# Kernel tuning notes

Measured on AMD Instinct MI355X. Metric: run time of the kernel, lower is better.

Reference implementation:

```python
import jax, jax.numpy as jnp
import numpy as np

B, PATCH, S, D, LAYERS, TOP_K, N_HEADS = 32, 196, 77, 512, 2, 16, 8


def setup_inputs() -> dict:
    key = jax.random.key(0)
    ks = jax.random.split(key, 16)
    d, L = D, LAYERS
    attn_std = d ** -0.5
    proj_std = (d ** -0.5) * ((2 * L) ** -0.5)
    fc_std = (2 * d) ** -0.5
    scale = d ** -0.5
    f = jnp.float32
    return {
        'image_feature': jax.random.normal(ks[0], (B, d), f),
        'image_tokens': jax.random.normal(ks[1], (B, PATCH, d), f),
        'text_feature': jax.random.normal(ks[2], (B, d), f),
        'text_tokens': jax.random.normal(ks[3], (B, S, d), f),
        'atte_mask': jax.random.randint(ks[4], (B, S), 0, 2).astype(jnp.int32),
        'img_cls': scale * jax.random.normal(ks[5], (d,), f),
        'txt_cls': scale * jax.random.normal(ks[6], (d,), f),
        'in_proj_w': attn_std * jax.random.normal(ks[7], (L, 3 * d, d), f),
        'in_proj_b': jnp.zeros((L, 3 * d), f),
        'out_w': proj_std * jax.random.normal(ks[8], (L, d, d), f),
        'out_b': jnp.zeros((L, d), f),
        'ln1_w': jnp.ones((L, d), f), 'ln1_b': jnp.zeros((L, d), f),
        'ln2_w': jnp.ones((L, d), f), 'ln2_b': jnp.zeros((L, d), f),
        'ln3_w': jnp.ones((L, d), f), 'ln3_b': jnp.zeros((L, d), f),
        'fc_w': fc_std * jax.random.normal(ks[9], (L, 4 * d, d), f),
        'fc_b': jnp.zeros((L, 4 * d), f),
        'proj_w': proj_std * jax.random.normal(ks[10], (L, d, 4 * d), f),
        'proj_b': jnp.zeros((L, d), f),
    }


def _ln(x, w, b):
    m = jnp.mean(x, axis=-1, keepdims=True)
    v = jnp.mean((x - m) ** 2, axis=-1, keepdims=True)
    return (x - m) * jax.lax.rsqrt(v + 1e-5) * w + b


def _mha(q, k, wi, bi, wo, bo):
    # q: (N, Lq, d), k: (N, Lk, d)
    N, Lq, d = q.shape
    hd = d // N_HEADS
    qh = (q @ wi[:d].T + bi[:d]).reshape(N, Lq, N_HEADS, hd)
    kh = (k @ wi[d:2 * d].T + bi[d:2 * d]).reshape(N, -1, N_HEADS, hd)
    vh = (k @ wi[2 * d:].T + bi[2 * d:]).reshape(N, -1, N_HEADS, hd)
    att = jax.nn.softmax(jnp.einsum('bqhd,bkhd->bhqk', qh, kh) * (hd ** -0.5), axis=-1)
    o = jnp.einsum('bhqk,bkhd->bqhd', att, vh).reshape(N, Lq, d)
    return o @ wo.T + bo


def _cross_attention(q4, k4, p):
    shape4 = q4.shape
    q = q4.reshape(-1, q4.shape[-2], q4.shape[-1])
    k = k4.reshape(-1, k4.shape[-2], k4.shape[-1])
    for i in range(LAYERS):
        kn = _ln(k, p['ln2_w'][i], p['ln2_b'][i])
        q = q + _mha(_ln(q, p['ln1_w'][i], p['ln1_b'][i]), kn,
                     p['in_proj_w'][i], p['in_proj_b'][i], p['out_w'][i], p['out_b'][i])
        h = _ln(q, p['ln3_w'][i], p['ln3_b'][i]) @ p['fc_w'][i].T + p['fc_b'][i]
        h = h * jax.nn.sigmoid(1.702 * h)  # QuickGELU
        q = q + h @ p['proj_w'][i].T + p['proj_b'][i]
    return q.reshape(shape4)


def _forward(image_feature, image_tokens, text_feature, text_tokens, atte_mask,
             img_cls, txt_cls, p):
    b, patch, d = image_tokens.shape
    s = text_tokens.shape[1]
    img_n = image_tokens / jnp.linalg.norm(image_tokens, axis=-1, keepdims=True)
    txt_n = text_tokens / jnp.linalg.norm(text_tokens, axis=-1, keepdims=True)
    # pairwise token similarities: (b_img, b_txt, patch, s)
    sim = jnp.einsum('ipd,jsd->ijps', img_n, txt_n)
    img_scores = jnp.einsum('ijps,js->ijp', sim, atte_mask.astype(sim.dtype))
    txt_scores = sim.sum(axis=2)  # (b, b, s)
    # top-k; torch scatter+masked_select gathers in ascending index order
    idx_i = jnp.sort(jax.lax.top_k(img_scores, TOP_K)[1], axis=-1)  # (b,b,k)
    idx_t = jnp.sort(jax.lax.top_k(txt_scores, TOP_K)[1], axis=-1)
    img_sel = img_n[jnp.arange(b)[:, None, None], idx_i]  # (b,b,k,d)
    txt_sel = txt_n[jnp.arange(b)[None, :, None], idx_t]  # (b,b,k,d)
    img_feat = jnp.broadcast_to(image_feature[:, None, None, :], (b, b, 1, d))
    txt_feat = jnp.broadcast_to(text_feature[None, :, None, :], (b, b, 1, d))
    img_cls4 = jnp.broadcast_to(img_cls, (b, b, 1, d))
    txt_cls4 = jnp.broadcast_to(txt_cls, (b, b, 1, d))
    final_img = _cross_attention(jnp.concatenate([img_cls4, img_sel], axis=2),
                                 jnp.concatenate([txt_feat, txt_sel], axis=2), p)
    final_txt = _cross_attention(jnp.concatenate([txt_cls4, txt_sel], axis=2),
                                 jnp.concatenate([img_feat, img_sel], axis=2), p)
    return final_img, final_txt


def reference(image_feature, image_tokens, text_feature, text_tokens, atte_mask,
              img_cls, txt_cls, in_proj_w, in_proj_b, out_w, out_b,
              ln1_w, ln1_b, ln2_w, ln2_b, ln3_w, ln3_b,
              fc_w, fc_b, proj_w, proj_b):
    p = dict(in_proj_w=in_proj_w, in_proj_b=in_proj_b, out_w=out_w, out_b=out_b,
             ln1_w=ln1_w, ln1_b=ln1_b, ln2_w=ln2_w, ln2_b=ln2_b,
             ln3_w=ln3_w, ln3_b=ln3_b, fc_w=fc_w, fc_b=fc_b,
             proj_w=proj_w, proj_b=proj_b)
    return _forward(image_feature, image_tokens, text_feature, text_tokens,
                    atte_mask, img_cls, txt_cls, p)
```

## Files before the change

### kernel.cpp

```cpp
#include <hip/hip_runtime.h>
#include <hip/hip_bf16.h>
#include <stdint.h>


typedef __attribute__((ext_vector_type(8))) short short8;
typedef __attribute__((ext_vector_type(4))) float f32x4;

__device__ __forceinline__ float bf2f(short u) {
    return __uint_as_float(((uint32_t)(uint16_t)u) << 16);
}
__device__ __forceinline__ unsigned short f2bf(float f) {
    __hip_bfloat16 h = __float2bfloat16(f);
    return *reinterpret_cast<unsigned short*>(&h);
}
__device__ __forceinline__ void gload16(const void* g, void* l) {
    __builtin_amdgcn_global_load_lds(
        (const __attribute__((address_space(1))) unsigned int*)g,
        (__attribute__((address_space(3))) unsigned int*)l, 16, 0, 0);
}

__global__ __launch_bounds__(256) void k_f2b(const float* __restrict__ in,
                                             unsigned short* __restrict__ out, int n) {
    for (int i = blockIdx.x * 256 + threadIdx.x; i < n; i += gridDim.x * 256)
        out[i] = f2bf(in[i]);
}

__global__ __launch_bounds__(256) void k_l2norm(const float* __restrict__ in,
                                                float* __restrict__ out) {
    size_t row = blockIdx.x;
    const float* x = in + row * 512;
    int t = threadIdx.x;
    float a0 = x[t], a1 = x[t + 256];
    float ss = a0 * a0 + a1 * a1;
#pragma unroll
    for (int off = 32; off; off >>= 1) ss += __shfl_xor(ss, off);
    __shared__ float s4[4];
    if ((t & 63) == 0) s4[t >> 6] = ss;
    __syncthreads();
    float tot = s4[0] + s4[1] + s4[2] + s4[3];
    float inv = 1.0f / sqrtf(tot);
    out[row * 512 + t] = a0 * inv;
    out[row * 512 + t + 256] = a1 * inv;
}

__global__ __launch_bounds__(512) void k_colsum(const float* __restrict__ tok,
                                                const int* __restrict__ mask,
                                                float* __restrict__ out, int R) {
    int b = blockIdx.x;
    int d = threadIdx.x;
    float acc = 0.f;
    for (int r = 0; r < R; r++) {
        float m = mask ? (float)mask[b * R + r] : 1.f;
        acc += m * tok[((size_t)b * R + r) * 512 + d];
    }
    out[b * 512 + d] = acc;
}

__global__ __launch_bounds__(256) void k_scores(const float* __restrict__ tok,
                                                const float* __restrict__ vec,
                                                float* __restrict__ out, int R, int swap) {
    int bid = blockIdx.x;
    int i = bid >> 5, j = bid & 31;
    int tb = swap ? j : i;
    int vb = swap ? i : j;
    __shared__ float sv[512];
    for (int t = threadIdx.x; t < 512; t += 256) sv[t] = vec[vb * 512 + t];
    __syncthreads();
    int wv = threadIdx.x >> 6, lane = threadIdx.x & 63;
    for (int r = wv; r < R; r += 4) {
        const float* tr = tok + ((size_t)tb * R + r) * 512;
        float acc = 0.f;
#pragma unroll
        for (int c = 0; c < 8; c++) {
            int d = lane + c * 64;
            acc += tr[d] * sv[d];
        }
#pragma unroll
        for (int off = 32; off; off >>= 1) acc += __shfl_xor(acc, off);
        if (lane == 0) out[(size_t)bid * R + r] = acc;
    }
}

__global__ __launch_bounds__(64) void k_topk(const float* __restrict__ simg,
                                             const float* __restrict__ stxt,
                                             int* __restrict__ idx_i, int* __restrict__ idx_t) {
    int bid = blockIdx.x;
    bool isimg = bid < 1024;
    int ij = isimg ? bid : bid - 1024;
    const float* s = isimg ? simg + (size_t)ij * 196 : stxt + (size_t)ij * 77;
    int n = isimg ? 196 : 77;
    int* out = (isimg ? idx_i : idx_t) + ij * 16;
    int lane = threadIdx.x;
    float v[4];
    int ids[4];
#pragma unroll
    for (int k = 0; k < 4; k++) {
        int id = lane + k * 64;
        ids[k] = id;
        v[k] = (id < n) ? s[id] : -3.0e38f;
    }
    __shared__ int sel[16];
    for (int r = 0; r < 16; r++) {
        float bv = v[0];
        int bi = ids[0];
#pragma unroll
        for (int k = 1; k < 4; k++)
            if (v[k] > bv) { bv = v[k]; bi = ids[k]; }
#pragma unroll
        for (int off = 32; off; off >>= 1) {
            float ov = __shfl_xor(bv, off);
            int oi = __shfl_xor(bi, off);
            if (ov > bv || (ov == bv && oi < bi)) { bv = ov; bi = oi; }
        }
        if (lane == 0) sel[r] = bi;
#pragma unroll
        for (int k = 0; k < 4; k++)
            if (ids[k] == bi) v[k] = -3.0e38f;
    }
    if (lane == 0) {
        for (int a = 1; a < 16; a++) {
            int key = sel[a];
            int b = a - 1;
            while (b >= 0 && sel[b] > key) { sel[b + 1] = sel[b]; b--; }
            sel[b + 1] = key;
        }
        for (int a = 0; a < 16; a++) out[a] = sel[a];
    }
}

__global__ __launch_bounds__(128) void k_gather(const float* __restrict__ img_n,
                                                const float* __restrict__ txt_n,
                                                const float* __restrict__ img_feat,
                                                const float* __restrict__ txt_feat,
                                                const float* __restrict__ img_cls,
                                                const float* __restrict__ txt_cls,
                                                const int* __restrict__ idx_i,
                                                const int* __restrict__ idx_t,
                                                float* __restrict__ q,
                                                unsigned short* __restrict__ k) {
    int rid = blockIdx.x;
    int buf = rid / 34816;
    int rem = rid % 34816;
    int seq = rem / 17, t = rem % 17;
    int c = seq >> 10, ij = seq & 1023, i = ij >> 5, j = ij & 31;
    const float* src;
    if (buf == 0) {
        if (c == 0)
            src = (t == 0) ? img_cls : img_n + ((size_t)i * 196 + idx_i[ij * 16 + t - 1]) * 512;
        else
            src = (t == 0) ? txt_cls : txt_n + ((size_t)j * 77 + idx_t[ij * 16 + t - 1]) * 512;
    } else {
        if (c == 0)
            src = (t == 0) ? (txt_feat + (size_t)j * 512)
                           : txt_n + ((size_t)j * 77 + idx_t[ij * 16 + t - 1]) * 512;
        else
            src = (t == 0) ? (img_feat + (size_t)i * 512)
                           : img_n + ((size_t)i * 196 + idx_i[ij * 16 + t - 1]) * 512;
    }
    float4 v = ((const float4*)src)[threadIdx.x];
    size_t row = (size_t)seq * 17 + t;
    if (buf == 0) {
        ((float4*)(q + row * 512))[threadIdx.x] = v;
    } else {
        ushort4 o;
        o.x = f2bf(v.x); o.y = f2bf(v.y); o.z = f2bf(v.z); o.w = f2bf(v.w);
        ((ushort4*)(k + row * 512))[threadIdx.x] = o;
    }
}

template <int BF>
__global__ __launch_bounds__(256) void k_ln(const void* __restrict__ xv,
                                            const float* __restrict__ w,
                                            const float* __restrict__ b,
                                            unsigned short* __restrict__ out) {
    size_t row = blockIdx.x;
    int t = threadIdx.x;
    float a0, a1;
    if (BF) {
        const short* xr = (const short*)xv + row * 512;
        a0 = bf2f(xr[t]);
        a1 = bf2f(xr[t + 256]);
    } else {
        const float* xr = (const float*)xv + row * 512;
        a0 = xr[t];
        a1 = xr[t + 256];
    }
    float s = a0 + a1, qq = a0 * a0 + a1 * a1;
#pragma unroll
    for (int off = 32; off; off >>= 1) {
        s += __shfl_xor(s, off);
        qq += __shfl_xor(qq, off);
    }
    __shared__ float s4[4], q4[4];
    if ((t & 63) == 0) { s4[t >> 6] = s; q4[t >> 6] = qq; }
    __syncthreads();
    s = s4[0] + s4[1] + s4[2] + s4[3];
    qq = q4[0] + q4[1] + q4[2] + q4[3];
    float mean = s * (1.f / 512.f);
    float var = qq * (1.f / 512.f) - mean * mean;
    float rs = rsqrtf(var + 1e-5f);
    out[row * 512 + t] = f2bf((a0 - mean) * rs * w[t] + b[t]);
    out[row * 512 + t + 256] = f2bf((a1 - mean) * rs * w[t + 256] + b[t + 256]);
}

template <int MODE>
__global__ __launch_bounds__(256) void k_gemm(const unsigned short* __restrict__ A,
                                              const unsigned short* __restrict__ W,
                                              const float* __restrict__ bias,
                                              void* __restrict__ Cv, int K, int ldc, int nxt) {
    __shared__ __align__(16) short sU[2][8192];

    int nwg = gridDim.x;
    int orig = blockIdx.x;
    int q8 = nwg >> 3, r8 = nwg & 7;
    int xcd = orig & 7, base = orig >> 3;
    int swz = (xcd < r8 ? xcd * (q8 + 1) : r8 * (q8 + 1) + (xcd - r8) * q8) + base;
    int tn = swz % nxt, tm = swz / nxt;

    int tid = threadIdx.x;
    int lane = tid & 63;
    int w = tid >> 6;
    int wm = w >> 1, wn = w & 1;
    int r16 = lane & 15, g = lane >> 4;

    int srow = tid >> 2;
    int sgran = tid & 3;
    int gchunk = (sgran ^ ((srow ^ (srow >> 2)) & 3)) * 8;
    const short* gA = (const short*)A + ((size_t)tm * 128 + srow) * K + gchunk;
    const short* gB = (const short*)W + ((size_t)tn * 128 + srow) * K + gchunk;
    int ldst = tid * 8;

    f32x4 acc[4][4] = {};
    int NU = K >> 5;

#define STAGE_UNIT(U, S)                                              \
    do {                                                              \
        size_t ko_ = (size_t)(U) * 32;                                \
        gload16(gA + ko_, &sU[(S)][ldst]);                            \
        gload16(gA + (size_t)64 * K + ko_, &sU[(S)][2048 + ldst]);    \
        gload16(gB + ko_, &sU[(S)][4096 + ldst]);                     \
        gload16(gB + (size_t)64 * K + ko_, &sU[(S)][6144 + ldst]);    \
    } while (0)

    STAGE_UNIT(0, 0);
    STAGE_UNIT(1, 1);

    int s = 0;
    for (int u = 0; u < NU; ++u) {
        if (u + 1 < NU) asm volatile("s_waitcnt vmcnt(4)" ::: "memory");
        else            asm volatile("s_waitcnt vmcnt(0)" ::: "memory");
        __builtin_amdgcn_s_barrier();
        __builtin_amdgcn_sched_barrier(0);

        const short* SA = &sU[s][0];
        const short* SB = &sU[s][4096];
        short8 a[4], b[4];
#pragma unroll
        for (int m = 0; m < 4; m++) {
            int row = wm * 64 + m * 16 + r16;
            a[m] = *(const short8*)&SA[row * 32 + ((g ^ ((row ^ (row >> 2)) & 3)) << 3)];
        }
#pragma unroll
        for (int n = 0; n < 4; n++) {
            int row = wn * 64 + n * 16 + r16;
            b[n] = *(const short8*)&SB[row * 32 + ((g ^ ((row ^ (row >> 2)) & 3)) << 3)];
        }
        __builtin_amdgcn_s_setprio(1);
#pragma unroll
        for (int m = 0; m < 4; m++)
#pragma unroll
            for (int n = 0; n < 4; n++)
                acc[m][n] = __builtin_amdgcn_mfma_f32_16x16x32_bf16(a[m], b[n], acc[m][n], 0, 0, 0);
        __builtin_amdgcn_s_setprio(0);
        __builtin_amdgcn_sched_barrier(0);
        __builtin_amdgcn_s_barrier();
        if (u + 2 < NU) STAGE_UNIT(u + 2, s);
        s ^= 1;
    }
#undef STAGE_UNIT

    size_t rbase = (size_t)tm * 128 + wm * 64 + g * 4;
    size_t cbase = (size_t)tn * 128 + wn * 64 + r16;
#pragma unroll
    for (int m = 0; m < 4; m++)
#pragma unroll
        for (int n = 0; n < 4; n++) {
            size_t col = cbase + n * 16;
            float bv = bias ? bias[col] : 0.f;
#pragma unroll
            for (int r = 0; r < 4; r++) {
                size_t row = rbase + m * 16 + r;
                float val = acc[m][n][r] + bv;
                if (MODE == 0) {
                    ((unsigned short*)Cv)[row * ldc + col] = f2bf(val);
                } else if (MODE == 1) {
                    float gv = val / (1.f + __expf(-1.702f * val));
                    ((unsigned short*)Cv)[row * ldc + col] = f2bf(gv);
                } else {
                    ((float*)Cv)[row * ldc + col] += val;
                }
            }
        }
}

__global__ __launch_bounds__(512) void k_attn(const unsigned short* __restrict__ Qm,
                                              const unsigned short* __restrict__ KVm,
                                              unsigned short* __restrict__ Om) {
    __shared__ __align__(16) short sAll[3 * 17 * 520];
    __shared__ float sP[8 * 17 * 17];
    int seq = blockIdx.x;
    size_t tb = (size_t)seq * 17;
    for (int c = threadIdx.x; c < 3264; c += 512) {
        int mat = c / 1088, rem = c % 1088, row = rem >> 6, ch = rem & 63;
        const short8* src;
        if (mat == 0)
            src = (const short8*)(Qm + (tb + row) * 512 + ch * 8);
        else if (mat == 1)
            src = (const short8*)(KVm + (tb + row) * 1024 + ch * 8);
        else
            src = (const short8*)(KVm + (tb + row) * 1024 + 512 + ch * 8);
        *(short8*)&sAll[mat * (17 * 520) + row * 520 + ch * 8] = *src;
    }
    __syncthreads();
    int h = threadIdx.x >> 6, lane = threadIdx.x & 63;
    const short* sQ = sAll;
    const short* sK = sAll + 17 * 520;
    const short* sV = sAll + 2 * 17 * 520;
    int jj = lane < 17 ? lane : 0;
    for (int i = 0; i < 17; i++) {
        float acc = 0.f;
#pragma unroll
        for (int c = 0; c < 8; c++) {
            short8 q8 = *(const short8*)&sQ[i * 520 + h * 64 + c * 8];
            short8 k8 = *(const short8*)&sK[jj * 520 + h * 64 + c * 8];
#pragma unroll
            for (int e = 0; e < 8; e++) acc += bf2f(q8[e]) * bf2f(k8[e]);
        }
        float sc = (lane < 17) ? acc * 0.125f : -1e30f;
        float m = sc;
#pragma unroll
        for (int off = 32; off; off >>= 1) m = fmaxf(m, __shfl_xor(m, off));
        float p = (lane < 17) ? __expf(sc - m) : 0.f;
        float sum = p;
#pragma unroll
        for (int off = 32; off; off >>= 1) sum += __shfl_xor(sum, off);
        if (lane < 17) sP[(h * 17 + i) * 17 + lane] = p / sum;
    }
    for (int i = 0; i < 17; i++) {
        float o = 0.f;
#pragma unroll
        for (int t = 0; t < 17; t++)
            o += sP[(h * 17 + i) * 17 + t] * bf2f(sV[t * 520 + h * 64 + lane]);
        Om[(tb + i) * 512 + h * 64 + lane] = f2bf(o);
    }
}

extern "C" void kernel_launch(void* const* d_in, const int* in_sizes, int n_in,
                              void* d_out, int out_size, void* d_ws, size_t ws_size,
                              hipStream_t stream) {
    const float* image_feature = (const float*)d_in[0];
    const float* image_tokens = (const float*)d_in[1];
    const float* text_feature = (const float*)d_in[2];
    const float* text_tokens = (const float*)d_in[3];
    const int* atte_mask = (const int*)d_in[4];
    const float* img_cls = (const float*)d_in[5];
    const float* txt_cls = (const float*)d_in[6];
    const float* in_proj_w = (const float*)d_in[7];
    const float* in_proj_b = (const float*)d_in[8];
    const float* out_w = (const float*)d_in[9];
    const float* out_b = (const float*)d_in[10];
    const float* ln1_w = (const float*)d_in[11];
    const float* ln1_b = (const float*)d_in[12];
    const float* ln2_w = (const float*)d_in[13];
    const float* ln2_b = (const float*)d_in[14];
    const float* ln3_w = (const float*)d_in[15];
    const float* ln3_b = (const float*)d_in[16];
    const float* fc_w = (const float*)d_in[17];
    const float* fc_b = (const float*)d_in[18];
    const float* proj_w = (const float*)d_in[19];
    const float* proj_b = (const float*)d_in[20];

    char* ws = (char*)d_ws;
    const size_t OFF_K = 12582912;
    const size_t OFF_CH = OFF_K + 35651584;
    size_t avail = ws_size > OFF_CH ? ws_size - OFF_CH : 0;
    int C = 2048;
    while (C > 256 && (size_t)87040 * C > avail) C >>= 1;
    int nch = 2048 / C;

    unsigned short* wbf = (unsigned short*)ws;
    unsigned short* w_inproj = wbf;
    unsigned short* w_outp = wbf + 1572864;
    unsigned short* w_fc = wbf + 2097152;
    unsigned short* w_proj = wbf + 4194304;
    unsigned short* kstream = (unsigned short*)(ws + OFF_K);
    char* chreg = ws + OFF_CH;
    float* img_n = (float*)(chreg + 0);
    float* txt_n = (float*)(chreg + 12845056);
    float* isum = (float*)(chreg + 17891328);
    float* tmask = (float*)(chreg + 17956864);
    float* simg = (float*)(chreg + 18022400);
    float* stxt = (float*)(chreg + 18825216);
    int* idx_i = (int*)(chreg + 19140608);
    int* idx_t = (int*)(chreg + 19206144);
    unsigned short* qn = (unsigned short*)chreg;
    unsigned short* qkvQ = (unsigned short*)(chreg + (size_t)17408 * C);
    unsigned short* qkvKV = (unsigned short*)(chreg + (size_t)34816 * C);
    unsigned short* atto = (unsigned short*)(chreg + (size_t)69632 * C);
    unsigned short* hbuf = qkvQ;
    float* q = (float*)d_out;

    k_f2b<<<1024, 256, 0, stream>>>(in_proj_w, w_inproj, 1572864);
    k_f2b<<<1024, 256, 0, stream>>>(out_w, w_outp, 524288);
    k_f2b<<<1024, 256, 0, stream>>>(fc_w, w_fc, 2097152);
    k_f2b<<<1024, 256, 0, stream>>>(proj_w, w_proj, 2097152);

    k_l2norm<<<6272, 256, 0, stream>>>(image_tokens, img_n);
    k_l2norm<<<2464, 256, 0, stream>>>(text_tokens, txt_n);

    k_colsum<<<32, 512, 0, stream>>>(img_n, nullptr, isum, 196);
    k_colsum<<<32, 512, 0, stream>>>(txt_n, atte_mask, tmask, 77);

    k_scores<<<1024, 256, 0, stream>>>(img_n, tmask, simg, 196, 0);
    k_scores<<<1024, 256, 0, stream>>>(txt_n, isum, stxt, 77, 1);
    k_topk<<<2048, 64, 0, stream>>>(simg, stxt, idx_i, idx_t);
    k_gather<<<69632, 128, 0, stream>>>(img_n, txt_n, image_feature, text_feature,
                                        img_cls, txt_cls, idx_i, idx_t, q, kstream);

    for (int ch = 0; ch < nch; ch++) {
        size_t r0 = (size_t)ch * C * 17;
        float* qc = q + r0 * 512;
        const unsigned short* kc = kstream + r0 * 512;
        int rowsC = 17 * C;
        int gmt = rowsC / 128;
        for (int l = 0; l < 2; l++) {
            const unsigned short* Wq = w_inproj + (size_t)l * 786432;
            const unsigned short* Wkv = Wq + 262144;
            const float* bq = in_proj_b + l * 1536;
            const float* bkv = bq + 512;
            k_ln<0><<<rowsC, 256, 0, stream>>>(qc, ln1_w + l * 512, ln1_b + l * 512, qn);
            k_gemm<0><<<gmt * 4, 256, 0, stream>>>(qn, Wq, bq, qkvQ, 512, 512, 4);
            k_ln<1><<<rowsC, 256, 0, stream>>>(kc, ln2_w + l * 512, ln2_b + l * 512, qn);
            k_gemm<0><<<gmt * 8, 256, 0, stream>>>(qn, Wkv, bkv, qkvKV, 512, 1024, 8);
            k_attn<<<C, 512, 0, stream>>>(qkvQ, qkvKV, atto);
            k_gemm<2><<<gmt * 4, 256, 0, stream>>>(atto, w_outp + (size_t)l * 262144,
                                                   out_b + l * 512, qc, 512, 512, 4);
            k_ln<0><<<rowsC, 256, 0, stream>>>(qc, ln3_w + l * 512, ln3_b + l * 512, qn);
            k_gemm<1><<<gmt * 16, 256, 0, stream>>>(qn, w_fc + (size_t)l * 1048576,
                                                    fc_b + l * 2048, hbuf, 512, 2048, 16);
            k_gemm<2><<<gmt * 4, 256, 0, stream>>>(hbuf, w_proj + (size_t)l * 1048576,
                                                   proj_b + l * 512, qc, 2048, 512, 4);
        }
    }
}
```

Measured before the change: 1.352 ms.

## Use 256x128 GEMM tiles and split-K with atomics for residual GEMMs

Enlarges the GEMM tile from 128x128 to 256x128 so each block computes 8x4 MFMA fragments per wave, which reuses every loaded weight tile across twice as many rows. This halves the number of M tiles. To keep enough blocks for the narrow N=512 residual GEMMs (out-proj and MLP proj), it adds a split-K of 2 that accumulates into the fp32 residual with atomicAdd, adding the bias only in the first split. The costs are more accumulator registers and LDS per block, atomic traffic, a nondeterministic summation order, and the requirement that the row count be a multiple of 256.

```diff
diff --git a/kernel.cpp b/kernel.cpp
--- a/kernel.cpp
+++ b/kernel.cpp
@@ -207,15 +207,19 @@
 __global__ __launch_bounds__(256) void k_gemm(const unsigned short* __restrict__ A,
                                               const unsigned short* __restrict__ W,
                                               const float* __restrict__ bias,
-                                              void* __restrict__ Cv, int K, int ldc, int nxt) {
-    __shared__ __align__(16) short sU[2][8192];
+                                              void* __restrict__ Cv, int K, int lda,
+                                              int ldc, int nxt, int nsplit) {
+    __shared__ __align__(16) short sU[2][12288];
 
     int nwg = gridDim.x;
     int orig = blockIdx.x;
     int q8 = nwg >> 3, r8 = nwg & 7;
     int xcd = orig & 7, base = orig >> 3;
     int swz = (xcd < r8 ? xcd * (q8 + 1) : r8 * (q8 + 1) + (xcd - r8) * q8) + base;
-    int tn = swz % nxt, tm = swz / nxt;
+    int tps = nwg / nsplit;
+    int sp = swz / tps;
+    int rem = swz % tps;
+    int tn = rem % nxt, tm = rem / nxt;
 
     int tid = threadIdx.x;
     int lane = tid & 63;
@@ -226,20 +230,22 @@
     int srow = tid >> 2;
     int sgran = tid & 3;
     int gchunk = (sgran ^ ((srow ^ (srow >> 2)) & 3)) * 8;
-    const short* gA = (const short*)A + ((size_t)tm * 128 + srow) * K + gchunk;
-    const short* gB = (const short*)W + ((size_t)tn * 128 + srow) * K + gchunk;
+    const short* gA = (const short*)A + (size_t)sp * K + ((size_t)tm * 256 + srow) * lda + gchunk;
+    const short* gB = (const short*)W + (size_t)sp * K + ((size_t)tn * 128 + srow) * lda + gchunk;
     int ldst = tid * 8;
 
-    f32x4 acc[4][4] = {};
+    f32x4 acc[8][4] = {};
     int NU = K >> 5;
 
-#define STAGE_UNIT(U, S)                                              \
-    do {                                                              \
-        size_t ko_ = (size_t)(U) * 32;                                \
-        gload16(gA + ko_, &sU[(S)][ldst]);                            \
-        gload16(gA + (size_t)64 * K + ko_, &sU[(S)][2048 + ldst]);    \
-        gload16(gB + ko_, &sU[(S)][4096 + ldst]);                     \
-        gload16(gB + (size_t)64 * K + ko_, &sU[(S)][6144 + ldst]);    \
+#define STAGE_UNIT(U, S)                                                   \
+    do {                                                                   \
+        size_t ko_ = (size_t)(U) * 32;                                     \
+        gload16(gA + ko_, &sU[(S)][ldst]);                                 \
+        gload16(gA + (size_t)64 * lda + ko_, &sU[(S)][2048 + ldst]);       \
+        gload16(gA + (size_t)128 * lda + ko_, &sU[(S)][4096 + ldst]);      \
+        gload16(gA + (size_t)192 * lda + ko_, &sU[(S)][6144 + ldst]);      \
+        gload16(gB + ko_, &sU[(S)][8192 + ldst]);                          \
+        gload16(gB + (size_t)64 * lda + ko_, &sU[(S)][10240 + ldst]);      \
     } while (0)
 
     STAGE_UNIT(0, 0);
@@ -247,27 +253,27 @@
 
     int s = 0;
     for (int u = 0; u < NU; ++u) {
-        if (u + 1 < NU) asm volatile("s_waitcnt vmcnt(4)" ::: "memory");
+        if (u + 1 < NU) asm volatile("s_waitcnt vmcnt(6)" ::: "memory");
         else            asm volatile("s_waitcnt vmcnt(0)" ::: "memory");
         __builtin_amdgcn_s_barrier();
         __builtin_amdgcn_sched_barrier(0);
 
         const short* SA = &sU[s][0];
-        const short* SB = &sU[s][4096];
-        short8 a[4], b[4];
-#pragma unroll
-        for (int m = 0; m < 4; m++) {
-            int row = wm * 64 + m * 16 + r16;
-            a[m] = *(const short8*)&SA[row * 32 + ((g ^ ((row ^ (row >> 2)) & 3)) << 3)];
-        }
+        const short* SB = &sU[s][8192];
+        short8 a[8], b[4];
 #pragma unroll
         for (int n = 0; n < 4; n++) {
             int row = wn * 64 + n * 16 + r16;
             b[n] = *(const short8*)&SB[row * 32 + ((g ^ ((row ^ (row >> 2)) & 3)) << 3)];
         }
+#pragma unroll
+        for (int m = 0; m < 8; m++) {
+            int row = wm * 128 + m * 16 + r16;
+            a[m] = *(const short8*)&SA[row * 32 + ((g ^ ((row ^ (row >> 2)) & 3)) << 3)];
+        }
         __builtin_amdgcn_s_setprio(1);
 #pragma unroll
-        for (int m = 0; m < 4; m++)
+        for (int m = 0; m < 8; m++)
 #pragma unroll
             for (int n = 0; n < 4; n++)
                 acc[m][n] = __builtin_amdgcn_mfma_f32_16x16x32_bf16(a[m], b[n], acc[m][n], 0, 0, 0);
@@ -279,14 +285,14 @@
     }
 #undef STAGE_UNIT
 
-    size_t rbase = (size_t)tm * 128 + wm * 64 + g * 4;
+    size_t rbase = (size_t)tm * 256 + wm * 128 + g * 4;
     size_t cbase = (size_t)tn * 128 + wn * 64 + r16;
 #pragma unroll
-    for (int m = 0; m < 4; m++)
+    for (int m = 0; m < 8; m++)
 #pragma unroll
         for (int n = 0; n < 4; n++) {
             size_t col = cbase + n * 16;
-            float bv = bias ? bias[col] : 0.f;
+            float bv = (bias && sp == 0) ? bias[col] : 0.f;
 #pragma unroll
             for (int r = 0; r < 4; r++) {
                 size_t row = rbase + m * 16 + r;
@@ -296,8 +302,10 @@
                 } else if (MODE == 1) {
                     float gv = val / (1.f + __expf(-1.702f * val));
                     ((unsigned short*)Cv)[row * ldc + col] = f2bf(gv);
+                } else if (MODE == 2) {
+                    ((float*)Cv)[row * ldc + col] += val;
                 } else {
-                    ((float*)Cv)[row * ldc + col] += val;
+                    atomicAdd(&((float*)Cv)[row * ldc + col], val);
                 }
             }
         }
@@ -432,24 +440,29 @@
         float* qc = q + r0 * 512;
         const unsigned short* kc = kstream + r0 * 512;
         int rowsC = 17 * C;
-        int gmt = rowsC / 128;
+        int gmt = rowsC / 256;
         for (int l = 0; l < 2; l++) {
             const unsigned short* Wq = w_inproj + (size_t)l * 786432;
             const unsigned short* Wkv = Wq + 262144;
             const float* bq = in_proj_b + l * 1536;
             const float* bkv = bq + 512;
             k_ln<0><<<rowsC, 256, 0, stream>>>(qc, ln1_w + l * 512, ln1_b + l * 512, qn);
-            k_gemm<0><<<gmt * 4, 256, 0, stream>>>(qn, Wq, bq, qkvQ, 512, 512, 4);
+            k_gemm<0><<<gmt * 4, 256, 0, stream>>>(qn, Wq, bq, qkvQ,
+                                                   512, 512, 512, 4, 1);
             k_ln<1><<<rowsC, 256, 0, stream>>>(kc, ln2_w + l * 512, ln2_b + l * 512, qn);
-            k_gemm<0><<<gmt * 8, 256, 0, stream>>>(qn, Wkv, bkv, qkvKV, 512, 1024, 8);
+            k_gemm<0><<<gmt * 8, 256, 0, stream>>>(qn, Wkv, bkv, qkvKV,
+                                                   512, 512, 1024, 8, 1);
             k_attn<<<C, 512, 0, stream>>>(qkvQ, qkvKV, atto);
-            k_gemm<2><<<gmt * 4, 256, 0, stream>>>(atto, w_outp + (size_t)l * 262144,
-                                                   out_b + l * 512, qc, 512, 512, 4);
+            k_gemm<3><<<gmt * 4 * 2, 256, 0, stream>>>(atto, w_outp + (size_t)l * 262144,
+                                                       out_b + l * 512, qc,
+                                                       256, 512, 512, 4, 2);
             k_ln<0><<<rowsC, 256, 0, stream>>>(qc, ln3_w + l * 512, ln3_b + l * 512, qn);
             k_gemm<1><<<gmt * 16, 256, 0, stream>>>(qn, w_fc + (size_t)l * 1048576,
-                                                    fc_b + l * 2048, hbuf, 512, 2048, 16);
-            k_gemm<2><<<gmt * 4, 256, 0, stream>>>(hbuf, w_proj + (size_t)l * 1048576,
-                                                   proj_b + l * 512, qc, 2048, 512, 4);
-        }
-    }
-}
+                                                    fc_b + l * 2048, hbuf,
+                                                    512, 512, 2048, 16, 1);
+            k_gemm<3><<<gmt * 4 * 2, 256, 0, stream>>>(hbuf, w_proj + (size_t)l * 1048576,
+                                                       proj_b + l * 512, qc,
+                                                       1024, 2048, 512, 4, 2);
+        }
+    }
+}
```

Measured after the change: 1.929 ms. +42.7%, slower.

## Use 2-wave 128x128 GEMM tiles and one-wave-per-row vectorized LayerNorm

Applied to the files above, without the earlier changes.

The GEMM drops from 4 waves of 64x64 subtiles to 2 waves that each compute a 128x64 subtile, so every wave reuses its B fragments across 8 A fragments. Each thread now issues 8 global-to-LDS loads per stage, and the kernel declares 2 blocks per CU in its launch bounds. LayerNorm is rewritten to handle one row per wavefront with 16-byte vector loads and stores, which removes the shared-memory reduction and the block barrier. The larger accumulator arrays raise register pressure and cut the number of waves per tile, which could reduce latency hiding.

```diff
diff --git a/kernel.cpp b/kernel.cpp
--- a/kernel.cpp
+++ b/kernel.cpp
@@ -173,41 +173,49 @@
                                             const float* __restrict__ w,
                                             const float* __restrict__ b,
                                             unsigned short* __restrict__ out) {
-    size_t row = blockIdx.x;
-    int t = threadIdx.x;
-    float a0, a1;
+    int wv = threadIdx.x >> 6, lane = threadIdx.x & 63;
+    size_t row = (size_t)blockIdx.x * 4 + wv;
+    float v[8];
     if (BF) {
-        const short* xr = (const short*)xv + row * 512;
-        a0 = bf2f(xr[t]);
-        a1 = bf2f(xr[t + 256]);
+        short8 x = *(const short8*)((const short*)xv + row * 512 + lane * 8);
+#pragma unroll
+        for (int e = 0; e < 8; e++) v[e] = bf2f(x[e]);
     } else {
-        const float* xr = (const float*)xv + row * 512;
-        a0 = xr[t];
-        a1 = xr[t + 256];
-    }
-    float s = a0 + a1, qq = a0 * a0 + a1 * a1;
+        const float* xr = (const float*)xv + row * 512 + lane * 8;
+        float4 x0 = *(const float4*)xr;
+        float4 x1 = *(const float4*)(xr + 4);
+        v[0] = x0.x; v[1] = x0.y; v[2] = x0.z; v[3] = x0.w;
+        v[4] = x1.x; v[5] = x1.y; v[6] = x1.z; v[7] = x1.w;
+    }
+    float s = 0.f, qq = 0.f;
+#pragma unroll
+    for (int e = 0; e < 8; e++) { s += v[e]; qq += v[e] * v[e]; }
 #pragma unroll
     for (int off = 32; off; off >>= 1) {
         s += __shfl_xor(s, off);
         qq += __shfl_xor(qq, off);
     }
-    __shared__ float s4[4], q4[4];
-    if ((t & 63) == 0) { s4[t >> 6] = s; q4[t >> 6] = qq; }
-    __syncthreads();
-    s = s4[0] + s4[1] + s4[2] + s4[3];
-    qq = q4[0] + q4[1] + q4[2] + q4[3];
     float mean = s * (1.f / 512.f);
     float var = qq * (1.f / 512.f) - mean * mean;
     float rs = rsqrtf(var + 1e-5f);
-    out[row * 512 + t] = f2bf((a0 - mean) * rs * w[t] + b[t]);
-    out[row * 512 + t + 256] = f2bf((a1 - mean) * rs * w[t + 256] + b[t + 256]);
+    const float* wr = w + lane * 8;
+    const float* br = b + lane * 8;
+    float4 w0 = *(const float4*)wr, w1 = *(const float4*)(wr + 4);
+    float4 b0 = *(const float4*)br, b1 = *(const float4*)(br + 4);
+    float wv8[8] = {w0.x, w0.y, w0.z, w0.w, w1.x, w1.y, w1.z, w1.w};
+    float bv8[8] = {b0.x, b0.y, b0.z, b0.w, b1.x, b1.y, b1.z, b1.w};
+    short8 res;
+#pragma unroll
+    for (int e = 0; e < 8; e++)
+        res[e] = (short)f2bf((v[e] - mean) * rs * wv8[e] + bv8[e]);
+    *(short8*)(out + row * 512 + lane * 8) = res;
 }
 
 template <int MODE>
-__global__ __launch_bounds__(256) void k_gemm(const unsigned short* __restrict__ A,
-                                              const unsigned short* __restrict__ W,
-                                              const float* __restrict__ bias,
-                                              void* __restrict__ Cv, int K, int ldc, int nxt) {
+__global__ __launch_bounds__(128, 2) void k_gemm(const unsigned short* __restrict__ A,
+                                                 const unsigned short* __restrict__ W,
+                                                 const float* __restrict__ bias,
+                                                 void* __restrict__ Cv, int K, int ldc, int nxt) {
     __shared__ __align__(16) short sU[2][8192];
 
     int nwg = gridDim.x;
@@ -220,26 +228,27 @@
     int tid = threadIdx.x;
     int lane = tid & 63;
     int w = tid >> 6;
-    int wm = w >> 1, wn = w & 1;
     int r16 = lane & 15, g = lane >> 4;
 
-    int srow = tid >> 2;
-    int sgran = tid & 3;
-    int gchunk = (sgran ^ ((srow ^ (srow >> 2)) & 3)) * 8;
-    const short* gA = (const short*)A + ((size_t)tm * 128 + srow) * K + gchunk;
-    const short* gB = (const short*)W + ((size_t)tn * 128 + srow) * K + gchunk;
-    int ldst = tid * 8;
-
-    f32x4 acc[4][4] = {};
+    int sr = (w << 4) + (lane >> 2);
+    int sg = lane & 3;
+    int sch = (sg ^ ((sr ^ (sr >> 2)) & 3)) * 8;
+    const short* gA = (const short*)A + ((size_t)tm * 128 + sr) * K + sch;
+    const short* gB = (const short*)W + ((size_t)tn * 128 + sr) * K + sch;
+
+    f32x4 acc[8][4] = {};
     int NU = K >> 5;
 
-#define STAGE_UNIT(U, S)                                              \
-    do {                                                              \
-        size_t ko_ = (size_t)(U) * 32;                                \
-        gload16(gA + ko_, &sU[(S)][ldst]);                            \
-        gload16(gA + (size_t)64 * K + ko_, &sU[(S)][2048 + ldst]);    \
-        gload16(gB + ko_, &sU[(S)][4096 + ldst]);                     \
-        gload16(gB + (size_t)64 * K + ko_, &sU[(S)][6144 + ldst]);    \
+#define STAGE_UNIT(U, S)                                                     \
+    do {                                                                     \
+        size_t ko_ = (size_t)(U) * 32;                                       \
+        _Pragma("unroll")                                                    \
+        for (int c_ = 0; c_ < 4; c_++) {                                     \
+            gload16(gA + (size_t)c_ * 32 * K + ko_,                          \
+                    &sU[(S)][c_ * 1024 + w * 512]);                          \
+            gload16(gB + (size_t)c_ * 32 * K + ko_,                          \
+                    &sU[(S)][4096 + c_ * 1024 + w * 512]);                   \
+        }                                                                    \
     } while (0)
 
     STAGE_UNIT(0, 0);
@@ -247,27 +256,27 @@
 
     int s = 0;
     for (int u = 0; u < NU; ++u) {
-        if (u + 1 < NU) asm volatile("s_waitcnt vmcnt(4)" ::: "memory");
+        if (u + 1 < NU) asm volatile("s_waitcnt vmcnt(8)" ::: "memory");
         else            asm volatile("s_waitcnt vmcnt(0)" ::: "memory");
         __builtin_amdgcn_s_barrier();
         __builtin_amdgcn_sched_barrier(0);
 
         const short* SA = &sU[s][0];
         const short* SB = &sU[s][4096];
-        short8 a[4], b[4];
-#pragma unroll
-        for (int m = 0; m < 4; m++) {
-            int row = wm * 64 + m * 16 + r16;
+        short8 a[8], b[4];
+#pragma unroll
+        for (int n = 0; n < 4; n++) {
+            int row = w * 64 + n * 16 + r16;
+            b[n] = *(const short8*)&SB[row * 32 + ((g ^ ((row ^ (row >> 2)) & 3)) << 3)];
+        }
+#pragma unroll
+        for (int m = 0; m < 8; m++) {
+            int row = m * 16 + r16;
             a[m] = *(const short8*)&SA[row * 32 + ((g ^ ((row ^ (row >> 2)) & 3)) << 3)];
         }
-#pragma unroll
-        for (int n = 0; n < 4; n++) {
-            int row = wn * 64 + n * 16 + r16;
-            b[n] = *(const short8*)&SB[row * 32 + ((g ^ ((row ^ (row >> 2)) & 3)) << 3)];
-        }
         __builtin_amdgcn_s_setprio(1);
 #pragma unroll
-        for (int m = 0; m < 4; m++)
+        for (int m = 0; m < 8; m++)
 #pragma unroll
             for (int n = 0; n < 4; n++)
                 acc[m][n] = __builtin_amdgcn_mfma_f32_16x16x32_bf16(a[m], b[n], acc[m][n], 0, 0, 0);
@@ -279,10 +288,10 @@
     }
 #undef STAGE_UNIT
 
-    size_t rbase = (size_t)tm * 128 + wm * 64 + g * 4;
-    size_t cbase = (size_t)tn * 128 + wn * 64 + r16;
-#pragma unroll
-    for (int m = 0; m < 4; m++)
+    size_t rbase = (size_t)tm * 128 + g * 4;
+    size_t cbase = (size_t)tn * 128 + w * 64 + r16;
+#pragma unroll
+    for (int m = 0; m < 8; m++)
 #pragma unroll
         for (int n = 0; n < 4; n++) {
             size_t col = cbase + n * 16;
@@ -433,22 +442,23 @@
         const unsigned short* kc = kstream + r0 * 512;
         int rowsC = 17 * C;
         int gmt = rowsC / 128;
+        int gln = rowsC / 4;
         for (int l = 0; l < 2; l++) {
             const unsigned short* Wq = w_inproj + (size_t)l * 786432;
             const unsigned short* Wkv = Wq + 262144;
             const float* bq = in_proj_b + l * 1536;
             const float* bkv = bq + 512;
-            k_ln<0><<<rowsC, 256, 0, stream>>>(qc, ln1_w + l * 512, ln1_b + l * 512, qn);
-            k_gemm<0><<<gmt * 4, 256, 0, stream>>>(qn, Wq, bq, qkvQ, 512, 512, 4);
-            k_ln<1><<<rowsC, 256, 0, stream>>>(kc, ln2_w + l * 512, ln2_b + l * 512, qn);
-            k_gemm<0><<<gmt * 8, 256, 0, stream>>>(qn, Wkv, bkv, qkvKV, 512, 1024, 8);
+            k_ln<0><<<gln, 256, 0, stream>>>(qc, ln1_w + l * 512, ln1_b + l * 512, qn);
+            k_gemm<0><<<gmt * 4, 128, 0, stream>>>(qn, Wq, bq, qkvQ, 512, 512, 4);
+            k_ln<1><<<gln, 256, 0, stream>>>(kc, ln2_w + l * 512, ln2_b + l * 512, qn);
+            k_gemm<0><<<gmt * 8, 128, 0, stream>>>(qn, Wkv, bkv, qkvKV, 512, 1024, 8);
             k_attn<<<C, 512, 0, stream>>>(qkvQ, qkvKV, atto);
-            k_gemm<2><<<gmt * 4, 256, 0, stream>>>(atto, w_outp + (size_t)l * 262144,
+            k_gemm<2><<<gmt * 4, 128, 0, stream>>>(atto, w_outp + (size_t)l * 262144,
                                                    out_b + l * 512, qc, 512, 512, 4);
-            k_ln<0><<<rowsC, 256, 0, stream>>>(qc, ln3_w + l * 512, ln3_b + l * 512, qn);
-            k_gemm<1><<<gmt * 16, 256, 0, stream>>>(qn, w_fc + (size_t)l * 1048576,
+            k_ln<0><<<gln, 256, 0, stream>>>(qc, ln3_w + l * 512, ln3_b + l * 512, qn);
+            k_gemm<1><<<gmt * 16, 128, 0, stream>>>(qn, w_fc + (size_t)l * 1048576,
                                                     fc_b + l * 2048, hbuf, 512, 2048, 16);
-            k_gemm<2><<<gmt * 4, 256, 0, stream>>>(hbuf, w_proj + (size_t)l * 1048576,
+            k_gemm<2><<<gmt * 4, 128, 0, stream>>>(hbuf, w_proj + (size_t)l * 1048576,
                                                    proj_b + l * 512, qc, 2048, 512, 4);
         }
     }
```

Measured after the change: 1.489 ms. 10.2% more time.
